# Kernel tuning notes

Hardware: AMD Instinct MI355X
Metric: run time of the kernel (lower is better)

The kernel has to match this reference:

```python
import jax, jax.numpy as jnp
import numpy as np

N = 100000        # nodes
E = 1600000       # edges (avg degree 16)
IN_C = 128
HID = 128
OUT_C = 18


def setup_inputs() -> dict:
    key = jax.random.key(0)
    k_x, k_e, k_w1, k_b1, k_w2, k_b2 = jax.random.split(key, 6)
    x = jax.random.normal(k_x, (N, IN_C), dtype=jnp.float32)
    edge_index = jax.random.randint(k_e, (2, E), 0, N, dtype=jnp.int64)
    # Glorot-ish init for linear weights, zero bias (PyG GCNConv defaults)
    W1 = jax.random.normal(k_w1, (IN_C, HID), dtype=jnp.float32) / np.sqrt(IN_C)
    b1 = jnp.zeros((HID,), dtype=jnp.float32)
    W2 = jax.random.normal(k_w2, (HID, OUT_C), dtype=jnp.float32) / np.sqrt(HID)
    b2 = jnp.zeros((OUT_C,), dtype=jnp.float32)
    return {"x": x, "edge_index": edge_index, "W1": W1, "b1": b1, "W2": W2, "b2": b2}


def _gcn_conv(x, src, dst, norm, W, b, n_nodes):
    # PyG GCNConv: linear transform, then normalized scatter-add aggregation
    h = x @ W                                   # [N, d_out]
    msg = h[src] * norm[:, None]                # gather + scale: [E+N, d_out]
    out = jax.ops.segment_sum(msg, dst, num_segments=n_nodes)
    return out + b


def reference(x, edge_index, W1, b1, W2, b2):
    src, dst = edge_index[0], edge_index[1]
    loop = jnp.arange(N, dtype=edge_index.dtype)
    src_f = jnp.concatenate([src, loop])        # add self-loops
    dst_f = jnp.concatenate([dst, loop])
    # symmetric normalization deg^-1/2[src] * deg^-1/2[dst] (with self-loops)
    deg = jax.ops.segment_sum(jnp.ones_like(dst_f, dtype=x.dtype), dst_f, num_segments=N)
    dinv = jnp.where(deg > 0, jax.lax.rsqrt(deg), 0.0)
    norm = dinv[src_f] * dinv[dst_f]            # [E+N]

    h = _gcn_conv(x, src_f, dst_f, norm, W1, b1, N)
    h = jax.nn.relu(h)
    # dropout is identity in eval mode (training=False)
    h = _gcn_conv(h, src_f, dst_f, norm, W2, b2, N)
    return jax.nn.log_softmax(h, axis=1)
```

## Files before the change

### kernel.cpp

```cpp
#include <hip/hip_runtime.h>
#include <math.h>

#define NN 100000
#define NE 1600000
#define CH  128
#define CO  18
#define NPB 256
#define NBUK ((NN + NPB - 1) / NPB)
#define EPB 4096
#define NBB ((NE + EPB - 1) / EPB)

typedef unsigned int uint;
typedef unsigned short ushort;
typedef float floatx4 __attribute__((ext_vector_type(4)));
typedef short short8 __attribute__((ext_vector_type(8)));
typedef ushort ushort4v __attribute__((ext_vector_type(4)));

__device__ __forceinline__ float bf_lo(uint u) { return __uint_as_float(u << 16); }
__device__ __forceinline__ float bf_hi(uint u) { return __uint_as_float(u & 0xFFFF0000u); }
__device__ __forceinline__ ushort f2bf(float f) {
    uint u = __float_as_uint(f);
    u += 0x7FFFu + ((u >> 16) & 1u);
    return (ushort)(u >> 16);
}
__device__ __forceinline__ uint pack_bf16(float a, float b) {
    return (uint)f2bf(a) | ((uint)f2bf(b) << 16);
}


union FatLDS {
    int h[NBUK];
    struct { ushort As[128 * 128]; ushort Bs[128 * 128]; } g;
};

__global__ __launch_bounds__(256, 2) void k_fat1(const int* __restrict__ dst,
                                                 int* __restrict__ bcnt,
                                                 const float* __restrict__ x,
                                                 const float* __restrict__ W1,
                                                 ushort* __restrict__ h1s) {
    __shared__ FatLDS L;
    int tid = threadIdx.x;

    if (blockIdx.x < NBB) {
        for (int i = tid; i < NBUK; i += 256) L.h[i] = 0;
        __syncthreads();
        int e0 = blockIdx.x * EPB;
#pragma unroll
        for (int i = 0; i < EPB / 256; ++i) {
            int e = e0 + i * 256 + tid;
            if (e < NE) atomicAdd(&L.h[dst[e] >> 8], 1);
        }
        __syncthreads();
        for (int i = tid; i < NBUK; i += 256)
            if (L.h[i]) atomicAdd(&bcnt[i], L.h[i]);
        return;
    }

    int row0 = (blockIdx.x - NBB) * 128;

    for (int p = tid; p < 8192; p += 256) {
        int kp = p >> 7, n = p & 127;
        float w0 = W1[(2 * kp) * 128 + n];
        float w1 = W1[(2 * kp + 1) * 128 + n];
        ((uint*)L.g.Bs)[(n * 64 + kp) ^ ((n & 7) << 2)] = pack_bf16(w0, w1);
    }
    for (int i = 0; i < 16; ++i) {
        int flat = i * 256 + tid;
        int r = flat >> 5, c4 = flat & 31;
        int gr = row0 + r;
        float4 v = (gr < NN) ? ((const float4*)x)[(size_t)gr * 32 + c4]
                             : make_float4(0.f, 0.f, 0.f, 0.f);
        ushort4v p;
        p.x = f2bf(v.x); p.y = f2bf(v.y); p.z = f2bf(v.z); p.w = f2bf(v.w);
        int idx = (r * 128 + c4 * 4) ^ ((r & 7) << 3);
        *(ushort4v*)&L.g.As[idx] = p;
    }
    __syncthreads();

    int lane = tid & 63;
    int wave = tid >> 6;
    int wrow = wave * 32;
    int lr = lane & 15;
    int lk8 = (lane >> 4) * 8;

    floatx4 acc[2][8];
#pragma unroll
    for (int a = 0; a < 2; ++a)
#pragma unroll
        for (int b = 0; b < 8; ++b) acc[a][b] = (floatx4)(0.0f);

#pragma unroll
    for (int ks = 0; ks < 4; ++ks) {
        int k0 = ks * 32 + lk8;
        int r0r = wrow + lr;
        int r1r = wrow + 16 + lr;
        short8 a0 = *(const short8*)&L.g.As[(r0r * 128 + k0) ^ ((r0r & 7) << 3)];
        short8 a1 = *(const short8*)&L.g.As[(r1r * 128 + k0) ^ ((r1r & 7) << 3)];
#pragma unroll
        for (int nt = 0; nt < 8; ++nt) {
            int n = nt * 16 + lr;
            short8 bf = *(const short8*)&L.g.Bs[(n * 128 + k0) ^ ((n & 7) << 3)];
            acc[0][nt] = __builtin_amdgcn_mfma_f32_16x16x32_bf16(a0, bf, acc[0][nt], 0, 0, 0);
            acc[1][nt] = __builtin_amdgcn_mfma_f32_16x16x32_bf16(a1, bf, acc[1][nt], 0, 0, 0);
        }
    }

    int drow = (lane >> 4) * 4;
#pragma unroll
    for (int rt = 0; rt < 2; ++rt) {
#pragma unroll
        for (int i = 0; i < 4; ++i) {
            int gr = row0 + wrow + rt * 16 + drow + i;
            if (gr < NN) {
                size_t base = (size_t)gr * 128;
#pragma unroll
                for (int nt = 0; nt < 8; ++nt)
                    h1s[base + nt * 16 + lr] = f2bf(acc[rt][nt][i]);
            }
        }
    }
}


__global__ __launch_bounds__(512) void k_bscan(const int* __restrict__ bcnt,
                                               int* __restrict__ bbase,
                                               int* __restrict__ bcur) {
    __shared__ int s[512];
    int tid = threadIdx.x;
    int c = (tid < NBUK) ? bcnt[tid] : 0;
    s[tid] = c;
    __syncthreads();
    for (int off = 1; off < 512; off <<= 1) {
        int t = (tid >= off) ? s[tid - off] : 0;
        __syncthreads();
        s[tid] += t;
        __syncthreads();
    }
    if (tid < NBUK) {
        int ex = s[tid] - c;
        bbase[tid] = ex;
        bcur[tid] = ex;
    }
    if (tid == NBUK) bbase[NBUK] = NE;
}

__global__ __launch_bounds__(256) void k_bin(const int* __restrict__ src,
                                             const int* __restrict__ dst,
                                             int* __restrict__ bcur,
                                             uint* __restrict__ etmp) {
    __shared__ int h[NBUK];
    __shared__ int base[NBUK];
    int tid = threadIdx.x;
    for (int i = tid; i < NBUK; i += 256) h[i] = 0;
    __syncthreads();

    int e0 = blockIdx.x * EPB;
    int sv[EPB / 256], dv[EPB / 256];
#pragma unroll
    for (int i = 0; i < EPB / 256; ++i) {
        int e = e0 + i * 256 + tid;
        if (e < NE) {
            sv[i] = src[e];
            dv[i] = dst[e];
            atomicAdd(&h[dv[i] >> 8], 1);
        } else {
            dv[i] = -1;
        }
    }
    __syncthreads();
    for (int i = tid; i < NBUK; i += 256)
        base[i] = h[i] ? atomicAdd(&bcur[i], h[i]) : 0;
    __syncthreads();
    for (int i = tid; i < NBUK; i += 256) h[i] = 0;
    __syncthreads();
#pragma unroll
    for (int i = 0; i < EPB / 256; ++i) {
        if (dv[i] >= 0) {
            int b = dv[i] >> 8;
            int pos = base[b] + atomicAdd(&h[b], 1);
            etmp[pos] = ((uint)sv[i] << 8) | ((uint)dv[i] & 255u);
        }
    }
}

__global__ __launch_bounds__(256) void k_pass2(const int* __restrict__ bbase,
                                               const uint* __restrict__ etmp,
                                               int* __restrict__ row_start,
                                               float* __restrict__ dinv,
                                               int* __restrict__ csr_src) {
    __shared__ int hist[NPB];
    __shared__ int s[NPB];
    __shared__ int cur[NPB];
    int tid = threadIdx.x;
    int b = blockIdx.x;
    int e0 = bbase[b], e1 = bbase[b + 1];

    hist[tid] = 0;
    __syncthreads();
    for (int e = e0 + tid; e < e1; e += 256)
        atomicAdd(&hist[etmp[e] & 255u], 1);
    __syncthreads();

    int c = hist[tid];
    s[tid] = c;
    __syncthreads();
    for (int off = 1; off < 256; off <<= 1) {
        int t = (tid >= off) ? s[tid - off] : 0;
        __syncthreads();
        s[tid] += t;
        __syncthreads();
    }
    int pfx = s[tid] - c;
    s[tid] = pfx;
    cur[tid] = 0;

    int node = b * NPB + tid;
    if (node < NN) {
        row_start[node] = e0 + pfx;
        dinv[node] = rsqrtf((float)c + 1.0f);
    }
    if (b == NBUK - 1 && tid == 0) row_start[NN] = NE;
    __syncthreads();

    for (int e = e0 + tid; e < e1; e += 256) {
        uint r = etmp[e];
        int n = (int)(r & 255u);
        int p = e0 + s[n] + atomicAdd(&cur[n], 1);
        csr_src[p] = (int)(r >> 8);
    }
}


__global__ __launch_bounds__(128) void k_agg1(const int* __restrict__ row_start,
                                              const int* __restrict__ csr_src,
                                              const float* __restrict__ dinv,
                                              const uint* __restrict__ h1u,
                                              const float* __restrict__ b1,
                                              uint* __restrict__ h1ru) {
    int wave = threadIdx.x >> 6;
    int lane = threadIdx.x & 63;
    int i = blockIdx.x * 2 + wave;
    if (i >= NN) return;
    int r0 = row_start[i], r1 = row_start[i + 1];
    float di = dinv[i];
    float ax = 0.0f, ay = 0.0f;

    int j = r0;
    for (; j + 7 < r1; j += 8) {
        int s0 = csr_src[j],     s1 = csr_src[j + 1];
        int s2 = csr_src[j + 2], s3 = csr_src[j + 3];
        int s4 = csr_src[j + 4], s5 = csr_src[j + 5];
        int s6 = csr_src[j + 6], s7 = csr_src[j + 7];
        float w0 = dinv[s0] * di, w1 = dinv[s1] * di;
        float w2 = dinv[s2] * di, w3 = dinv[s3] * di;
        float w4 = dinv[s4] * di, w5 = dinv[s5] * di;
        float w6 = dinv[s6] * di, w7 = dinv[s7] * di;
        uint u0 = h1u[(size_t)s0 * 64 + lane];
        uint u1 = h1u[(size_t)s1 * 64 + lane];
        uint u2 = h1u[(size_t)s2 * 64 + lane];
        uint u3 = h1u[(size_t)s3 * 64 + lane];
        uint u4 = h1u[(size_t)s4 * 64 + lane];
        uint u5 = h1u[(size_t)s5 * 64 + lane];
        uint u6 = h1u[(size_t)s6 * 64 + lane];
        uint u7 = h1u[(size_t)s7 * 64 + lane];
        ax += w0 * bf_lo(u0) + w1 * bf_lo(u1) + w2 * bf_lo(u2) + w3 * bf_lo(u3)
            + w4 * bf_lo(u4) + w5 * bf_lo(u5) + w6 * bf_lo(u6) + w7 * bf_lo(u7);
        ay += w0 * bf_hi(u0) + w1 * bf_hi(u1) + w2 * bf_hi(u2) + w3 * bf_hi(u3)
            + w4 * bf_hi(u4) + w5 * bf_hi(u5) + w6 * bf_hi(u6) + w7 * bf_hi(u7);
    }
    for (; j < r1; ++j) {
        int s0 = csr_src[j];
        float w0 = dinv[s0] * di;
        uint u0 = h1u[(size_t)s0 * 64 + lane];
        ax += w0 * bf_lo(u0);
        ay += w0 * bf_hi(u0);
    }

    uint us = h1u[(size_t)i * 64 + lane];
    float2 bb = ((const float2*)b1)[lane];
    float di2 = di * di;
    float ox = fmaxf(ax + di2 * bf_lo(us) + bb.x, 0.0f);
    float oy = fmaxf(ay + di2 * bf_hi(us) + bb.y, 0.0f);
    h1ru[(size_t)i * 64 + lane] = pack_bf16(ox, oy);
}


__global__ __launch_bounds__(256, 2) void k_gemm2(const uint* __restrict__ h1ru,
                                                  const float* __restrict__ W2,
                                                  ushort* __restrict__ h2b) {
    __shared__ float xs[128][129];
    __shared__ float Ws[128 * 18];
    int row0 = blockIdx.x * 128;
    int tid = threadIdx.x;

    for (int i = tid; i < 128 * 18; i += 256) Ws[i] = W2[i];
    for (int i = tid; i < 128 * 64; i += 256) {
        int r = i >> 6, c2 = i & 63;
        int gr = row0 + r;
        uint u = (gr < NN) ? h1ru[(size_t)gr * 64 + c2] : 0u;
        xs[r][2 * c2]     = bf_lo(u);
        xs[r][2 * c2 + 1] = bf_hi(u);
    }
    __syncthreads();

    int rl   = tid & 127;
    int half = tid >> 7;
    int j0   = half * 9;
    float acc[9];
#pragma unroll
    for (int j = 0; j < 9; ++j) acc[j] = 0.0f;

#pragma unroll 4
    for (int k = 0; k < 128; ++k) {
        float xv = xs[rl][k];
#pragma unroll
        for (int j = 0; j < 9; ++j)
            acc[j] += xv * Ws[k * 18 + j0 + j];
    }
    int gr = row0 + rl;
    if (gr < NN) {
#pragma unroll
        for (int j = 0; j < 9; ++j)
            h2b[(size_t)gr * 24 + j0 + j] = f2bf(acc[j]);
        if (half) {
#pragma unroll
            for (int j = 0; j < 6; ++j)
                h2b[(size_t)gr * 24 + 18 + j] = 0;
        }
    }
}


__device__ __forceinline__ void acc6(float* acc, float wgt, uint4 av, uint2 cv) {
    acc[0]  += wgt * bf_lo(av.x); acc[1]  += wgt * bf_hi(av.x);
    acc[2]  += wgt * bf_lo(av.y); acc[3]  += wgt * bf_hi(av.y);
    acc[4]  += wgt * bf_lo(av.z); acc[5]  += wgt * bf_hi(av.z);
    acc[6]  += wgt * bf_lo(av.w); acc[7]  += wgt * bf_hi(av.w);
    acc[8]  += wgt * bf_lo(cv.x); acc[9]  += wgt * bf_hi(cv.x);
    acc[10] += wgt * bf_lo(cv.y); acc[11] += wgt * bf_hi(cv.y);
}

__global__ __launch_bounds__(256) void k_agg2(const int* __restrict__ row_start,
                                              const int* __restrict__ csr_src,
                                              const float* __restrict__ dinv,
                                              const uint* __restrict__ h2u,
                                              const float* __restrict__ b2,
                                              float* __restrict__ out) {
    int t = blockIdx.x * 256 + threadIdx.x;
    int i = t >> 1;
    int half = t & 1;
    if (i >= NN) return;
    int r0 = row_start[i], r1 = row_start[i + 1];
    float di = dinv[i];
    int base = half * 6;
    float acc[12];
#pragma unroll
    for (int j = 0; j < 12; ++j) acc[j] = 0.0f;

    int e = r0;
    for (; e + 3 < r1; e += 4) {
        int s0 = csr_src[e],     s1 = csr_src[e + 1];
        int s2 = csr_src[e + 2], s3 = csr_src[e + 3];
        float w0 = dinv[s0] * di, w1 = dinv[s1] * di;
        float w2 = dinv[s2] * di, w3 = dinv[s3] * di;
        const uint* p0 = h2u + (size_t)s0 * 12 + base;
        const uint* p1 = h2u + (size_t)s1 * 12 + base;
        const uint* p2 = h2u + (size_t)s2 * 12 + base;
        const uint* p3 = h2u + (size_t)s3 * 12 + base;
        uint4 a0 = *(const uint4*)p0; uint2 c0 = *(const uint2*)(p0 + 4);
        uint4 a1 = *(const uint4*)p1; uint2 c1 = *(const uint2*)(p1 + 4);
        uint4 a2 = *(const uint4*)p2; uint2 c2 = *(const uint2*)(p2 + 4);
        uint4 a3 = *(const uint4*)p3; uint2 c3 = *(const uint2*)(p3 + 4);
        acc6(acc, w0, a0, c0);
        acc6(acc, w1, a1, c1);
        acc6(acc, w2, a2, c2);
        acc6(acc, w3, a3, c3);
    }
    for (; e < r1; ++e) {
        int s = csr_src[e];
        float w = dinv[s] * di;
        const uint* p = h2u + (size_t)s * 12 + base;
        uint4 a = *(const uint4*)p; uint2 c = *(const uint2*)(p + 4);
        acc6(acc, w, a, c);
    }

    float di2 = di * di;
    const uint* pi = h2u + (size_t)i * 12 + base;
    uint4 ia = *(const uint4*)pi; uint2 ic = *(const uint2*)(pi + 4);
    acc6(acc, di2, ia, ic);

    int ch0 = half * 12;
    float m = -1e30f;
#pragma unroll
    for (int j = 0; j < 12; ++j) {
        int ch = ch0 + j;
        if (ch < CO) {
            acc[j] += b2[ch];
            m = fmaxf(m, acc[j]);
        }
    }
    m = fmaxf(m, __shfl_xor(m, 1));
    float sum = 0.0f;
#pragma unroll
    for (int j = 0; j < 12; ++j) {
        int ch = ch0 + j;
        if (ch < CO) sum += expf(acc[j] - m);
    }
    sum += __shfl_xor(sum, 1);
    float lse = logf(sum);
    float* op = out + (size_t)i * CO;
#pragma unroll
    for (int j = 0; j < 12; ++j) {
        int ch = ch0 + j;
        if (ch < CO) op[ch] = acc[j] - m - lse;
    }
}


extern "C" void kernel_launch(void* const* d_in, const int* in_sizes, int n_in,
                              void* d_out, int out_size, void* d_ws, size_t ws_size,
                              hipStream_t stream) {
    const float* x  = (const float*)d_in[0];
    const int*   ei = (const int*)d_in[1];
    const float* W1 = (const float*)d_in[2];
    const float* b1 = (const float*)d_in[3];
    const float* W2 = (const float*)d_in[4];
    const float* b2 = (const float*)d_in[5];
    float* out = (float*)d_out;

    const int* src = ei;
    const int* dst = ei + NE;

    uint* h1u  = (uint*)d_ws;
    uint* h1ru = h1u + (size_t)NN * 64;
    uint* h2u  = h1ru + (size_t)NN * 64;
    float* dinv = (float*)(h2u + (size_t)NN * 12);
    int* row_start = (int*)(dinv + NN);
    int* csr_src   = row_start + NN + 1;
    uint* etmp     = (uint*)(csr_src + NE);
    int* bcnt      = (int*)(etmp + NE);
    int* bbase     = bcnt + NBUK;
    int* bcur      = bbase + NBUK + 1;

    hipMemsetAsync(bcnt, 0, NBUK * sizeof(int), stream);

    k_fat1<<<NBB + (NN + 127) / 128, 256, 0, stream>>>(dst, bcnt, x, W1, (ushort*)h1u);
    k_bscan<<<1, 512, 0, stream>>>(bcnt, bbase, bcur);
    k_bin<<<NBB, 256, 0, stream>>>(src, dst, bcur, etmp);
    k_pass2<<<NBUK, 256, 0, stream>>>(bbase, etmp, row_start, dinv, csr_src);

    k_agg1<<<(NN + 1) / 2, 128, 0, stream>>>(row_start, csr_src, dinv, h1u, b1, h1ru);
    k_gemm2<<<(NN + 127) / 128, 256, 0, stream>>>(h1ru, W2, (ushort*)h2u);
    k_agg2<<<(2 * NN + 255) / 256, 256, 0, stream>>>(row_start, csr_src, dinv, h2u, b2, out);
}
```

Measured before the change: 255.4 us.

## Prescale features by source dinv and restructure degree counting before GEMM

```diff
diff --git a/kernel.cpp b/kernel.cpp
--- a/kernel.cpp
+++ b/kernel.cpp
@@ -28,31 +28,100 @@
 }
 
 
-union FatLDS {
-    int h[NBUK];
+__global__ __launch_bounds__(256) void k_count(const int* __restrict__ dst,
+                                               int* __restrict__ counts) {
+    int stride = gridDim.x * 256;
+    for (int e = blockIdx.x * 256 + threadIdx.x; e < NE; e += stride)
+        atomicAdd(&counts[dst[e]], 1);
+}
+
+
+__global__ __launch_bounds__(256) void k_dinv_bcnt(const int* __restrict__ counts,
+                                                   float* __restrict__ dinv,
+                                                   int* __restrict__ bcnt) {
+    __shared__ int s[256];
+    int tid = threadIdx.x;
+    int i = blockIdx.x * 256 + tid;
+    int c = (i < NN) ? counts[i] : 0;
+    if (i < NN) dinv[i] = rsqrtf((float)c + 1.0f);
+    s[tid] = c;
+    __syncthreads();
+    for (int off = 128; off > 0; off >>= 1) {
+        if (tid < off) s[tid] += s[tid + off];
+        __syncthreads();
+    }
+    if (tid == 0) bcnt[blockIdx.x] = s[0];
+}
+
+__global__ __launch_bounds__(512) void k_bscan(const int* __restrict__ bcnt,
+                                               int* __restrict__ bbase,
+                                               int* __restrict__ bcur) {
+    __shared__ int s[512];
+    int tid = threadIdx.x;
+    int c = (tid < NBUK) ? bcnt[tid] : 0;
+    s[tid] = c;
+    __syncthreads();
+    for (int off = 1; off < 512; off <<= 1) {
+        int t = (tid >= off) ? s[tid - off] : 0;
+        __syncthreads();
+        s[tid] += t;
+        __syncthreads();
+    }
+    if (tid < NBUK) {
+        int ex = s[tid] - c;
+        bbase[tid] = ex;
+        bcur[tid] = ex;
+    }
+    if (tid == NBUK) bbase[NBUK] = NE;
+}
+
+
+union FatBLDS {
+    struct { int h[NBUK]; int base[NBUK]; } b;
     struct { ushort As[128 * 128]; ushort Bs[128 * 128]; } g;
 };
 
-__global__ __launch_bounds__(256, 2) void k_fat1(const int* __restrict__ dst,
-                                                 int* __restrict__ bcnt,
+__global__ __launch_bounds__(256, 2) void k_fatB(const int* __restrict__ src,
+                                                 const int* __restrict__ dst,
+                                                 int* __restrict__ bcur,
+                                                 uint* __restrict__ etmp,
                                                  const float* __restrict__ x,
                                                  const float* __restrict__ W1,
+                                                 const float* __restrict__ dinv,
                                                  ushort* __restrict__ h1s) {
-    __shared__ FatLDS L;
+    __shared__ FatBLDS L;
     int tid = threadIdx.x;
 
     if (blockIdx.x < NBB) {
-        for (int i = tid; i < NBUK; i += 256) L.h[i] = 0;
+        for (int i = tid; i < NBUK; i += 256) L.b.h[i] = 0;
         __syncthreads();
         int e0 = blockIdx.x * EPB;
+        int sv[EPB / 256], dv[EPB / 256];
 #pragma unroll
         for (int i = 0; i < EPB / 256; ++i) {
             int e = e0 + i * 256 + tid;
-            if (e < NE) atomicAdd(&L.h[dst[e] >> 8], 1);
+            if (e < NE) {
+                sv[i] = src[e];
+                dv[i] = dst[e];
+                atomicAdd(&L.b.h[dv[i] >> 8], 1);
+            } else {
+                dv[i] = -1;
+            }
         }
         __syncthreads();
         for (int i = tid; i < NBUK; i += 256)
-            if (L.h[i]) atomicAdd(&bcnt[i], L.h[i]);
+            L.b.base[i] = L.b.h[i] ? atomicAdd(&bcur[i], L.b.h[i]) : 0;
+        __syncthreads();
+        for (int i = tid; i < NBUK; i += 256) L.b.h[i] = 0;
+        __syncthreads();
+#pragma unroll
+        for (int i = 0; i < EPB / 256; ++i) {
+            if (dv[i] >= 0) {
+                int b = dv[i] >> 8;
+                int pos = L.b.base[b] + atomicAdd(&L.b.h[b], 1);
+                etmp[pos] = ((uint)sv[i] << 8) | ((uint)dv[i] & 255u);
+            }
+        }
         return;
     }
 
@@ -112,96 +181,30 @@
         for (int i = 0; i < 4; ++i) {
             int gr = row0 + wrow + rt * 16 + drow + i;
             if (gr < NN) {
-                size_t base = (size_t)gr * 128;
+                float dv = dinv[gr];
+                uint base = (uint)gr * 128u;
 #pragma unroll
                 for (int nt = 0; nt < 8; ++nt)
-                    h1s[base + nt * 16 + lr] = f2bf(acc[rt][nt][i]);
+                    h1s[base + nt * 16 + lr] = f2bf(acc[rt][nt][i] * dv);
             }
         }
     }
 }
 
 
-__global__ __launch_bounds__(512) void k_bscan(const int* __restrict__ bcnt,
-                                               int* __restrict__ bbase,
-                                               int* __restrict__ bcur) {
-    __shared__ int s[512];
-    int tid = threadIdx.x;
-    int c = (tid < NBUK) ? bcnt[tid] : 0;
-    s[tid] = c;
-    __syncthreads();
-    for (int off = 1; off < 512; off <<= 1) {
-        int t = (tid >= off) ? s[tid - off] : 0;
-        __syncthreads();
-        s[tid] += t;
-        __syncthreads();
-    }
-    if (tid < NBUK) {
-        int ex = s[tid] - c;
-        bbase[tid] = ex;
-        bcur[tid] = ex;
-    }
-    if (tid == NBUK) bbase[NBUK] = NE;
-}
-
-__global__ __launch_bounds__(256) void k_bin(const int* __restrict__ src,
-                                             const int* __restrict__ dst,
-                                             int* __restrict__ bcur,
-                                             uint* __restrict__ etmp) {
-    __shared__ int h[NBUK];
-    __shared__ int base[NBUK];
-    int tid = threadIdx.x;
-    for (int i = tid; i < NBUK; i += 256) h[i] = 0;
-    __syncthreads();
-
-    int e0 = blockIdx.x * EPB;
-    int sv[EPB / 256], dv[EPB / 256];
-#pragma unroll
-    for (int i = 0; i < EPB / 256; ++i) {
-        int e = e0 + i * 256 + tid;
-        if (e < NE) {
-            sv[i] = src[e];
-            dv[i] = dst[e];
-            atomicAdd(&h[dv[i] >> 8], 1);
-        } else {
-            dv[i] = -1;
-        }
-    }
-    __syncthreads();
-    for (int i = tid; i < NBUK; i += 256)
-        base[i] = h[i] ? atomicAdd(&bcur[i], h[i]) : 0;
-    __syncthreads();
-    for (int i = tid; i < NBUK; i += 256) h[i] = 0;
-    __syncthreads();
-#pragma unroll
-    for (int i = 0; i < EPB / 256; ++i) {
-        if (dv[i] >= 0) {
-            int b = dv[i] >> 8;
-            int pos = base[b] + atomicAdd(&h[b], 1);
-            etmp[pos] = ((uint)sv[i] << 8) | ((uint)dv[i] & 255u);
-        }
-    }
-}
-
 __global__ __launch_bounds__(256) void k_pass2(const int* __restrict__ bbase,
+                                               const int* __restrict__ counts,
                                                const uint* __restrict__ etmp,
                                                int* __restrict__ row_start,
-                                               float* __restrict__ dinv,
                                                int* __restrict__ csr_src) {
-    __shared__ int hist[NPB];
     __shared__ int s[NPB];
     __shared__ int cur[NPB];
     int tid = threadIdx.x;
     int b = blockIdx.x;
     int e0 = bbase[b], e1 = bbase[b + 1];
 
-    hist[tid] = 0;
-    __syncthreads();
-    for (int e = e0 + tid; e < e1; e += 256)
-        atomicAdd(&hist[etmp[e] & 255u], 1);
-    __syncthreads();
-
-    int c = hist[tid];
+    int node = b * NPB + tid;
+    int c = (node < NN) ? counts[node] : 0;
     s[tid] = c;
     __syncthreads();
     for (int off = 1; off < 256; off <<= 1) {
@@ -214,11 +217,7 @@
     s[tid] = pfx;
     cur[tid] = 0;
 
-    int node = b * NPB + tid;
-    if (node < NN) {
-        row_start[node] = e0 + pfx;
-        dinv[node] = rsqrtf((float)c + 1.0f);
-    }
+    if (node < NN) row_start[node] = e0 + pfx;
     if (b == NBUK - 1 && tid == 0) row_start[NN] = NE;
     __syncthreads();
 
@@ -242,7 +241,6 @@
     int i = blockIdx.x * 2 + wave;
     if (i >= NN) return;
     int r0 = row_start[i], r1 = row_start[i + 1];
-    float di = dinv[i];
     float ax = 0.0f, ay = 0.0f;
 
     int j = r0;
@@ -251,42 +249,40 @@
         int s2 = csr_src[j + 2], s3 = csr_src[j + 3];
         int s4 = csr_src[j + 4], s5 = csr_src[j + 5];
         int s6 = csr_src[j + 6], s7 = csr_src[j + 7];
-        float w0 = dinv[s0] * di, w1 = dinv[s1] * di;
-        float w2 = dinv[s2] * di, w3 = dinv[s3] * di;
-        float w4 = dinv[s4] * di, w5 = dinv[s5] * di;
-        float w6 = dinv[s6] * di, w7 = dinv[s7] * di;
-        uint u0 = h1u[(size_t)s0 * 64 + lane];
-        uint u1 = h1u[(size_t)s1 * 64 + lane];
-        uint u2 = h1u[(size_t)s2 * 64 + lane];
-        uint u3 = h1u[(size_t)s3 * 64 + lane];
-        uint u4 = h1u[(size_t)s4 * 64 + lane];
-        uint u5 = h1u[(size_t)s5 * 64 + lane];
-        uint u6 = h1u[(size_t)s6 * 64 + lane];
-        uint u7 = h1u[(size_t)s7 * 64 + lane];
-        ax += w0 * bf_lo(u0) + w1 * bf_lo(u1) + w2 * bf_lo(u2) + w3 * bf_lo(u3)
-            + w4 * bf_lo(u4) + w5 * bf_lo(u5) + w6 * bf_lo(u6) + w7 * bf_lo(u7);
-        ay += w0 * bf_hi(u0) + w1 * bf_hi(u1) + w2 * bf_hi(u2) + w3 * bf_hi(u3)
-            + w4 * bf_hi(u4) + w5 * bf_hi(u5) + w6 * bf_hi(u6) + w7 * bf_hi(u7);
+        uint u0 = h1u[(uint)s0 * 64u + lane];
+        uint u1 = h1u[(uint)s1 * 64u + lane];
+        uint u2 = h1u[(uint)s2 * 64u + lane];
+        uint u3 = h1u[(uint)s3 * 64u + lane];
+        uint u4 = h1u[(uint)s4 * 64u + lane];
+        uint u5 = h1u[(uint)s5 * 64u + lane];
+        uint u6 = h1u[(uint)s6 * 64u + lane];
+        uint u7 = h1u[(uint)s7 * 64u + lane];
+        ax += (bf_lo(u0) + bf_lo(u1)) + (bf_lo(u2) + bf_lo(u3))
+            + (bf_lo(u4) + bf_lo(u5)) + (bf_lo(u6) + bf_lo(u7));
+        ay += (bf_hi(u0) + bf_hi(u1)) + (bf_hi(u2) + bf_hi(u3))
+            + (bf_hi(u4) + bf_hi(u5)) + (bf_hi(u6) + bf_hi(u7));
     }
     for (; j < r1; ++j) {
-        int s0 = csr_src[j];
-        float w0 = dinv[s0] * di;
-        uint u0 = h1u[(size_t)s0 * 64 + lane];
-        ax += w0 * bf_lo(u0);
-        ay += w0 * bf_hi(u0);
-    }
-
-    uint us = h1u[(size_t)i * 64 + lane];
+        uint u0 = h1u[(uint)csr_src[j] * 64u + lane];
+        ax += bf_lo(u0);
+        ay += bf_hi(u0);
+    }
+
+    uint us = h1u[(uint)i * 64u + lane];
+    ax += bf_lo(us);
+    ay += bf_hi(us);
+
+    float di = dinv[i];
     float2 bb = ((const float2*)b1)[lane];
-    float di2 = di * di;
-    float ox = fmaxf(ax + di2 * bf_lo(us) + bb.x, 0.0f);
-    float oy = fmaxf(ay + di2 * bf_hi(us) + bb.y, 0.0f);
-    h1ru[(size_t)i * 64 + lane] = pack_bf16(ox, oy);
+    float ox = fmaxf(ax * di + bb.x, 0.0f);
+    float oy = fmaxf(ay * di + bb.y, 0.0f);
+    h1ru[(uint)i * 64u + lane] = pack_bf16(ox, oy);
 }
 
 
 __global__ __launch_bounds__(256, 2) void k_gemm2(const uint* __restrict__ h1ru,
                                                   const float* __restrict__ W2,
+                                                  const float* __restrict__ dinv,
                                                   ushort* __restrict__ h2b) {
     __shared__ float xs[128][129];
     __shared__ float Ws[128 * 18];
@@ -297,7 +293,7 @@
     for (int i = tid; i < 128 * 64; i += 256) {
         int r = i >> 6, c2 = i & 63;
         int gr = row0 + r;
-        uint u = (gr < NN) ? h1ru[(size_t)gr * 64 + c2] : 0u;
+        uint u = (gr < NN) ? h1ru[(uint)gr * 64u + c2] : 0u;
         xs[r][2 * c2]     = bf_lo(u);
         xs[r][2 * c2 + 1] = bf_hi(u);
     }
@@ -319,25 +315,26 @@
     }
     int gr = row0 + rl;
     if (gr < NN) {
+        float dv = dinv[gr];
 #pragma unroll
         for (int j = 0; j < 9; ++j)
-            h2b[(size_t)gr * 24 + j0 + j] = f2bf(acc[j]);
+            h2b[(uint)gr * 24u + j0 + j] = f2bf(acc[j] * dv);
         if (half) {
 #pragma unroll
             for (int j = 0; j < 6; ++j)
-                h2b[(size_t)gr * 24 + 18 + j] = 0;
-        }
-    }
-}
-
-
-__device__ __forceinline__ void acc6(float* acc, float wgt, uint4 av, uint2 cv) {
-    acc[0]  += wgt * bf_lo(av.x); acc[1]  += wgt * bf_hi(av.x);
-    acc[2]  += wgt * bf_lo(av.y); acc[3]  += wgt * bf_hi(av.y);
-    acc[4]  += wgt * bf_lo(av.z); acc[5]  += wgt * bf_hi(av.z);
-    acc[6]  += wgt * bf_lo(av.w); acc[7]  += wgt * bf_hi(av.w);
-    acc[8]  += wgt * bf_lo(cv.x); acc[9]  += wgt * bf_hi(cv.x);
-    acc[10] += wgt * bf_lo(cv.y); acc[11] += wgt * bf_hi(cv.y);
+                h2b[(uint)gr * 24u + 18 + j] = 0;
+        }
+    }
+}
+
+
+__device__ __forceinline__ void add6(float* acc, uint4 av, uint2 cv) {
+    acc[0]  += bf_lo(av.x); acc[1]  += bf_hi(av.x);
+    acc[2]  += bf_lo(av.y); acc[3]  += bf_hi(av.y);
+    acc[4]  += bf_lo(av.z); acc[5]  += bf_hi(av.z);
+    acc[6]  += bf_lo(av.w); acc[7]  += bf_hi(av.w);
+    acc[8]  += bf_lo(cv.x); acc[9]  += bf_hi(cv.x);
+    acc[10] += bf_lo(cv.y); acc[11] += bf_hi(cv.y);
 }
 
 __global__ __launch_bounds__(256) void k_agg2(const int* __restrict__ row_start,
@@ -351,8 +348,7 @@
     int half = t & 1;
     if (i >= NN) return;
     int r0 = row_start[i], r1 = row_start[i + 1];
-    float di = dinv[i];
-    int base = half * 6;
+    uint base = (uint)half * 6u;
     float acc[12];
 #pragma unroll
     for (int j = 0; j < 12; ++j) acc[j] = 0.0f;
@@ -361,41 +357,37 @@
     for (; e + 3 < r1; e += 4) {
         int s0 = csr_src[e],     s1 = csr_src[e + 1];
         int s2 = csr_src[e + 2], s3 = csr_src[e + 3];
-        float w0 = dinv[s0] * di, w1 = dinv[s1] * di;
-        float w2 = dinv[s2] * di, w3 = dinv[s3] * di;
-        const uint* p0 = h2u + (size_t)s0 * 12 + base;
-        const uint* p1 = h2u + (size_t)s1 * 12 + base;
-        const uint* p2 = h2u + (size_t)s2 * 12 + base;
-        const uint* p3 = h2u + (size_t)s3 * 12 + base;
+        const uint* p0 = h2u + (uint)s0 * 12u + base;
+        const uint* p1 = h2u + (uint)s1 * 12u + base;
+        const uint* p2 = h2u + (uint)s2 * 12u + base;
+        const uint* p3 = h2u + (uint)s3 * 12u + base;
         uint4 a0 = *(const uint4*)p0; uint2 c0 = *(const uint2*)(p0 + 4);
         uint4 a1 = *(const uint4*)p1; uint2 c1 = *(const uint2*)(p1 + 4);
         uint4 a2 = *(const uint4*)p2; uint2 c2 = *(const uint2*)(p2 + 4);
         uint4 a3 = *(const uint4*)p3; uint2 c3 = *(const uint2*)(p3 + 4);
-        acc6(acc, w0, a0, c0);
-        acc6(acc, w1, a1, c1);
-        acc6(acc, w2, a2, c2);
-        acc6(acc, w3, a3, c3);
+        add6(acc, a0, c0);
+        add6(acc, a1, c1);
+        add6(acc, a2, c2);
+        add6(acc, a3, c3);
     }
     for (; e < r1; ++e) {
-        int s = csr_src[e];
-        float w = dinv[s] * di;
-        const uint* p = h2u + (size_t)s * 12 + base;
+        const uint* p = h2u + (uint)csr_src[e] * 12u + base;
         uint4 a = *(const uint4*)p; uint2 c = *(const uint2*)(p + 4);
-        acc6(acc, w, a, c);
-    }
-
-    float di2 = di * di;
-    const uint* pi = h2u + (size_t)i * 12 + base;
+        add6(acc, a, c);
+    }
+
+    const uint* pi = h2u + (uint)i * 12u + base;
     uint4 ia = *(const uint4*)pi; uint2 ic = *(const uint2*)(pi + 4);
-    acc6(acc, di2, ia, ic);
-
+    add6(acc, ia, ic);
+
+    float di = dinv[i];
     int ch0 = half * 12;
     float m = -1e30f;
 #pragma unroll
     for (int j = 0; j < 12; ++j) {
         int ch = ch0 + j;
         if (ch < CO) {
-            acc[j] += b2[ch];
+            acc[j] = acc[j] * di + b2[ch];
             m = fmaxf(m, acc[j]);
         }
     }
@@ -435,21 +427,24 @@
     uint* h1ru = h1u + (size_t)NN * 64;
     uint* h2u  = h1ru + (size_t)NN * 64;
     float* dinv = (float*)(h2u + (size_t)NN * 12);
-    int* row_start = (int*)(dinv + NN);
+    int* counts    = (int*)(dinv + NN);
+    int* row_start = counts + NN;
     int* csr_src   = row_start + NN + 1;
     uint* etmp     = (uint*)(csr_src + NE);
     int* bcnt      = (int*)(etmp + NE);
     int* bbase     = bcnt + NBUK;
     int* bcur      = bbase + NBUK + 1;
 
-    hipMemsetAsync(bcnt, 0, NBUK * sizeof(int), stream);
-
-    k_fat1<<<NBB + (NN + 127) / 128, 256, 0, stream>>>(dst, bcnt, x, W1, (ushort*)h1u);
+    hipMemsetAsync(counts, 0, (size_t)NN * sizeof(int), stream);
+
+    k_count<<<2048, 256, 0, stream>>>(dst, counts);
+    k_dinv_bcnt<<<NBUK, 256, 0, stream>>>(counts, dinv, bcnt);
     k_bscan<<<1, 512, 0, stream>>>(bcnt, bbase, bcur);
-    k_bin<<<NBB, 256, 0, stream>>>(src, dst, bcur, etmp);
-    k_pass2<<<NBUK, 256, 0, stream>>>(bbase, etmp, row_start, dinv, csr_src);
+    k_fatB<<<NBB + (NN + 127) / 128, 256, 0, stream>>>(src, dst, bcur, etmp,
+                                                       x, W1, dinv, (ushort*)h1u);
+    k_pass2<<<NBUK, 256, 0, stream>>>(bbase, counts, etmp, row_start, csr_src);
 
     k_agg1<<<(NN + 1) / 2, 128, 0, stream>>>(row_start, csr_src, dinv, h1u, b1, h1ru);
-    k_gemm2<<<(NN + 127) / 128, 256, 0, stream>>>(h1ru, W2, (ushort*)h2u);
+    k_gemm2<<<(NN + 127) / 128, 256, 0, stream>>>(h1ru, W2, dinv, (ushort*)h2u);
     k_agg2<<<(2 * NN + 255) / 256, 256, 0, stream>>>(row_start, csr_src, dinv, h2u, b2, out);
 }
```

New measurement: 296.8 us. 1.16x slower.

## Use one thread per node in layer-2 aggregation and 4 waves per agg1 block

Applied to the files above, without the earlier changes.

```diff
diff --git a/kernel.cpp b/kernel.cpp
--- a/kernel.cpp
+++ b/kernel.cpp
@@ -231,7 +231,7 @@
 }
 
 
-__global__ __launch_bounds__(128) void k_agg1(const int* __restrict__ row_start,
+__global__ __launch_bounds__(256) void k_agg1(const int* __restrict__ row_start,
                                               const int* __restrict__ csr_src,
                                               const float* __restrict__ dinv,
                                               const uint* __restrict__ h1u,
@@ -239,7 +239,7 @@
                                               uint* __restrict__ h1ru) {
     int wave = threadIdx.x >> 6;
     int lane = threadIdx.x & 63;
-    int i = blockIdx.x * 2 + wave;
+    int i = blockIdx.x * 4 + wave;
     if (i >= NN) return;
     int r0 = row_start[i], r1 = row_start[i + 1];
     float di = dinv[i];
@@ -322,22 +322,21 @@
 #pragma unroll
         for (int j = 0; j < 9; ++j)
             h2b[(size_t)gr * 24 + j0 + j] = f2bf(acc[j]);
-        if (half) {
-#pragma unroll
-            for (int j = 0; j < 6; ++j)
-                h2b[(size_t)gr * 24 + 18 + j] = 0;
-        }
-    }
-}
-
-
-__device__ __forceinline__ void acc6(float* acc, float wgt, uint4 av, uint2 cv) {
+    }
+}
+
+
+__device__ __forceinline__ void acc_row(float* acc, float wgt,
+                                        uint4 av, uint4 bv, uint cv) {
     acc[0]  += wgt * bf_lo(av.x); acc[1]  += wgt * bf_hi(av.x);
     acc[2]  += wgt * bf_lo(av.y); acc[3]  += wgt * bf_hi(av.y);
     acc[4]  += wgt * bf_lo(av.z); acc[5]  += wgt * bf_hi(av.z);
     acc[6]  += wgt * bf_lo(av.w); acc[7]  += wgt * bf_hi(av.w);
-    acc[8]  += wgt * bf_lo(cv.x); acc[9]  += wgt * bf_hi(cv.x);
-    acc[10] += wgt * bf_lo(cv.y); acc[11] += wgt * bf_hi(cv.y);
+    acc[8]  += wgt * bf_lo(bv.x); acc[9]  += wgt * bf_hi(bv.x);
+    acc[10] += wgt * bf_lo(bv.y); acc[11] += wgt * bf_hi(bv.y);
+    acc[12] += wgt * bf_lo(bv.z); acc[13] += wgt * bf_hi(bv.z);
+    acc[14] += wgt * bf_lo(bv.w); acc[15] += wgt * bf_hi(bv.w);
+    acc[16] += wgt * bf_lo(cv);   acc[17] += wgt * bf_hi(cv);
 }
 
 __global__ __launch_bounds__(256) void k_agg2(const int* __restrict__ row_start,
@@ -346,16 +345,13 @@
                                               const uint* __restrict__ h2u,
                                               const float* __restrict__ b2,
                                               float* __restrict__ out) {
-    int t = blockIdx.x * 256 + threadIdx.x;
-    int i = t >> 1;
-    int half = t & 1;
+    int i = blockIdx.x * 256 + threadIdx.x;
     if (i >= NN) return;
     int r0 = row_start[i], r1 = row_start[i + 1];
     float di = dinv[i];
-    int base = half * 6;
-    float acc[12];
-#pragma unroll
-    for (int j = 0; j < 12; ++j) acc[j] = 0.0f;
+    float acc[CO];
+#pragma unroll
+    for (int j = 0; j < CO; ++j) acc[j] = 0.0f;
 
     int e = r0;
     for (; e + 3 < r1; e += 4) {
@@ -363,57 +359,45 @@
         int s2 = csr_src[e + 2], s3 = csr_src[e + 3];
         float w0 = dinv[s0] * di, w1 = dinv[s1] * di;
         float w2 = dinv[s2] * di, w3 = dinv[s3] * di;
-        const uint* p0 = h2u + (size_t)s0 * 12 + base;
-        const uint* p1 = h2u + (size_t)s1 * 12 + base;
-        const uint* p2 = h2u + (size_t)s2 * 12 + base;
-        const uint* p3 = h2u + (size_t)s3 * 12 + base;
-        uint4 a0 = *(const uint4*)p0; uint2 c0 = *(const uint2*)(p0 + 4);
-        uint4 a1 = *(const uint4*)p1; uint2 c1 = *(const uint2*)(p1 + 4);
-        uint4 a2 = *(const uint4*)p2; uint2 c2 = *(const uint2*)(p2 + 4);
-        uint4 a3 = *(const uint4*)p3; uint2 c3 = *(const uint2*)(p3 + 4);
-        acc6(acc, w0, a0, c0);
-        acc6(acc, w1, a1, c1);
-        acc6(acc, w2, a2, c2);
-        acc6(acc, w3, a3, c3);
+        const uint* p0 = h2u + (size_t)s0 * 12;
+        const uint* p1 = h2u + (size_t)s1 * 12;
+        const uint* p2 = h2u + (size_t)s2 * 12;
+        const uint* p3 = h2u + (size_t)s3 * 12;
+        uint4 a0 = *(const uint4*)p0, b0 = *(const uint4*)(p0 + 4); uint c0 = p0[8];
+        uint4 a1 = *(const uint4*)p1, b1v = *(const uint4*)(p1 + 4); uint c1 = p1[8];
+        uint4 a2 = *(const uint4*)p2, b2v = *(const uint4*)(p2 + 4); uint c2 = p2[8];
+        uint4 a3 = *(const uint4*)p3, b3v = *(const uint4*)(p3 + 4); uint c3 = p3[8];
+        acc_row(acc, w0, a0, b0, c0);
+        acc_row(acc, w1, a1, b1v, c1);
+        acc_row(acc, w2, a2, b2v, c2);
+        acc_row(acc, w3, a3, b3v, c3);
     }
     for (; e < r1; ++e) {
         int s = csr_src[e];
         float w = dinv[s] * di;
-        const uint* p = h2u + (size_t)s * 12 + base;
-        uint4 a = *(const uint4*)p; uint2 c = *(const uint2*)(p + 4);
-        acc6(acc, w, a, c);
+        const uint* p = h2u + (size_t)s * 12;
+        uint4 a = *(const uint4*)p, b = *(const uint4*)(p + 4); uint c = p[8];
+        acc_row(acc, w, a, b, c);
     }
 
     float di2 = di * di;
-    const uint* pi = h2u + (size_t)i * 12 + base;
-    uint4 ia = *(const uint4*)pi; uint2 ic = *(const uint2*)(pi + 4);
-    acc6(acc, di2, ia, ic);
-
-    int ch0 = half * 12;
+    const uint* pi = h2u + (size_t)i * 12;
+    uint4 ia = *(const uint4*)pi, ib = *(const uint4*)(pi + 4); uint ic = pi[8];
+    acc_row(acc, di2, ia, ib, ic);
+
     float m = -1e30f;
 #pragma unroll
-    for (int j = 0; j < 12; ++j) {
-        int ch = ch0 + j;
-        if (ch < CO) {
-            acc[j] += b2[ch];
-            m = fmaxf(m, acc[j]);
-        }
-    }
-    m = fmaxf(m, __shfl_xor(m, 1));
+    for (int j = 0; j < CO; ++j) {
+        acc[j] += b2[j];
+        m = fmaxf(m, acc[j]);
+    }
     float sum = 0.0f;
 #pragma unroll
-    for (int j = 0; j < 12; ++j) {
-        int ch = ch0 + j;
-        if (ch < CO) sum += expf(acc[j] - m);
-    }
-    sum += __shfl_xor(sum, 1);
+    for (int j = 0; j < CO; ++j) sum += expf(acc[j] - m);
     float lse = logf(sum);
     float* op = out + (size_t)i * CO;
 #pragma unroll
-    for (int j = 0; j < 12; ++j) {
-        int ch = ch0 + j;
-        if (ch < CO) op[ch] = acc[j] - m - lse;
-    }
+    for (int j = 0; j < CO; ++j) op[j] = acc[j] - m - lse;
 }
 
 
@@ -449,7 +433,7 @@
     k_bin<<<NBB, 256, 0, stream>>>(src, dst, bcur, etmp);
     k_pass2<<<NBUK, 256, 0, stream>>>(bbase, etmp, row_start, dinv, csr_src);
 
-    k_agg1<<<(NN + 1) / 2, 128, 0, stream>>>(row_start, csr_src, dinv, h1u, b1, h1ru);
+    k_agg1<<<(NN + 3) / 4, 256, 0, stream>>>(row_start, csr_src, dinv, h1u, b1, h1ru);
     k_gemm2<<<(NN + 127) / 128, 256, 0, stream>>>(h1ru, W2, (ushort*)h2u);
-    k_agg2<<<(2 * NN + 255) / 256, 256, 0, stream>>>(row_start, csr_src, dinv, h2u, b2, out);
-}
+    k_agg2<<<(NN + 255) / 256, 256, 0, stream>>>(row_start, csr_src, dinv, h2u, b2, out);
+}
```

Result: faster. 249.0 us (-2.5%).
